# Kernel tuning notes

Hardware: AMD Instinct MI355X
Metric: run time of the kernel (lower is better)

## Reference

```python
import jax, jax.numpy as jnp
import numpy as np

D_MODEL = 768
N_HEADS = 12
HEAD_DIM = D_MODEL // N_HEADS


def setup_inputs() -> dict:
    key = jax.random.key(0)
    ks = jax.random.split(key, 7)
    B, S = 4, 2048
    scale = 1.0 / np.sqrt(D_MODEL)
    return {
        "hidden_states": jax.random.normal(ks[0], (B, S, D_MODEL), dtype=jnp.float32),
        "attention_mask": jnp.ones((B, S), dtype=jnp.float32),
        "Wq": jax.random.normal(ks[1], (D_MODEL, D_MODEL), dtype=jnp.float32) * scale,
        "bq": jnp.zeros((D_MODEL,), dtype=jnp.float32),
        "Wk": jax.random.normal(ks[2], (D_MODEL, D_MODEL), dtype=jnp.float32) * scale,
        "bk": jnp.zeros((D_MODEL,), dtype=jnp.float32),
        "Wv": jax.random.normal(ks[3], (D_MODEL, D_MODEL), dtype=jnp.float32) * scale,
        "bv": jnp.zeros((D_MODEL,), dtype=jnp.float32),
    }


def reference(hidden_states, attention_mask, Wq, bq, Wk, bk, Wv, bv):
    B, S, _ = hidden_states.shape

    def heads(x):  # [B,S,D] -> [B,H,S,hd]
        return x.reshape(B, S, N_HEADS, HEAD_DIM).transpose(0, 2, 1, 3)

    q = heads(hidden_states @ Wq + bq)
    k = heads(hidden_states @ Wk + bk)
    v = heads(hidden_states @ Wv + bv)

    # [B,H,S,S] scores -- explicitly materialized, as in the original module
    scores = jnp.einsum("bhqd,bhkd->bhqk", q, k) / np.sqrt(HEAD_DIM)
    mask_add = (1.0 - attention_mask)[:, None, None, :] * -10000.0
    scores = scores + mask_add
    probs = jax.nn.softmax(scores, axis=-1)  # dropout p=0 (eval) -> identity

    ctx = jnp.einsum("bhqk,bhkd->bhqd", probs, v)
    ctx = ctx.transpose(0, 2, 1, 3).reshape(B, S, D_MODEL)
    return ctx, probs
```

## Files before the change

### kernel.cpp

```cpp
#include <hip/hip_runtime.h>
#include <hip/hip_bf16.h>
#include <cstdint>

typedef short bf16x8 __attribute__((ext_vector_type(8)));
typedef float f32x4 __attribute__((ext_vector_type(4)));
typedef unsigned short ushort_t;

__device__ __forceinline__ ushort_t f2bf(float f) {
    uint32_t u = __float_as_uint(f);
    u = (u + 0x7fffu + ((u >> 16) & 1u)) >> 16;
    return (ushort_t)u;
}

__device__ __forceinline__ ushort_t f2bf_native(float f) {
    __hip_bfloat16 h = __float2bfloat16(f);
    return *reinterpret_cast<ushort_t*>(&h);
}

__device__ __forceinline__ void gl2lds16(const void* g, void* l) {
    __builtin_amdgcn_global_load_lds((const __attribute__((address_space(1))) void*)(g),
                                     (__attribute__((address_space(3))) void*)(l), 16, 0, 0);
}

__device__ __forceinline__ void wait_vm0() {
    asm volatile("s_waitcnt vmcnt(0)" ::: "memory");
}
__device__ __forceinline__ void wait_vm8() {
    asm volatile("s_waitcnt vmcnt(8)" ::: "memory");
}

__global__ void cvt_hidden(const float* __restrict__ in, ushort_t* __restrict__ out, int n4) {
    int i = blockIdx.x * blockDim.x + threadIdx.x;
    for (; i < n4; i += gridDim.x * blockDim.x) {
        float4 v = ((const float4*)in)[i];
        ushort_t tmp[4] __attribute__((aligned(8)));
        tmp[0] = f2bf(v.x); tmp[1] = f2bf(v.y); tmp[2] = f2bf(v.z); tmp[3] = f2bf(v.w);
        ((uint2*)out)[i] = *(uint2*)tmp;
    }
}

__global__ void wt_transpose(const float* __restrict__ Wq, const float* __restrict__ Wk,
                             const float* __restrict__ Wv, ushort_t* __restrict__ out) {
    __shared__ float tile[64][68];
    const float* W = blockIdx.z == 0 ? Wq : (blockIdx.z == 1 ? Wk : Wv);
    int k0 = blockIdx.x * 64, n0 = blockIdx.y * 64;
    int t = threadIdx.x;
    for (int i = 0; i < 4; ++i) {
        int e = i * 1024 + t * 4;
        int r = e >> 6, c = e & 63;
        float4 v = *(const float4*)(W + (k0 + r) * 768 + n0 + c);
        *(float4*)(&tile[r][c]) = v;
    }
    __syncthreads();
    ushort_t* o = out + blockIdx.z * 768 * 768;
    for (int i = 0; i < 2; ++i) {
        int e = i * 2048 + t * 8;
        int rn = e >> 6, ck = e & 63;
        ushort_t tmp[8] __attribute__((aligned(16)));
        for (int j = 0; j < 8; ++j) tmp[j] = f2bf(tile[ck + j][rn]);
        *(int4*)(o + (n0 + rn) * 768 + k0 + ck) = *(int4*)tmp;
    }
}

__launch_bounds__(256, 2)
__global__ void qkv_gemm(const ushort_t* __restrict__ A, const ushort_t* __restrict__ Wt,
                         const float* __restrict__ bq, const float* __restrict__ bk,
                         const float* __restrict__ bv,
                         ushort_t* __restrict__ q_out, ushort_t* __restrict__ k_out,
                         ushort_t* __restrict__ vt_out) {
    __shared__ char smem[65536];
    char* sA = smem;
    char* sB = smem + 32768;
    int z = blockIdx.z;
    const ushort_t* Wz = Wt + z * 589824;
    const float* bias = z == 0 ? bq : (z == 1 ? bk : bv);
    int m0 = blockIdx.x * 128, n0 = blockIdx.y * 128;
    int t = threadIdx.x, lane = t & 63, w = t >> 6;
    int wr = w >> 1, wc = w & 1;
    int lr = lane & 15, lg = lane >> 4;
    int rsub = lane >> 3;
    int jsw  = ((lane & 7) ^ rsub) * 8;

#pragma unroll
    for (int i = 0; i < 4; ++i) {
        int r = i * 32 + w * 8 + rsub;
        gl2lds16(A + (m0 + r) * 768 + jsw, sA + i * 4096 + w * 1024);
        gl2lds16(Wz + (n0 + r) * 768 + jsw, sB + i * 4096 + w * 1024);
    }
    wait_vm0();
    __syncthreads();

    f32x4 acc[4][4] = {};
    int cur = 0;
    for (int ktile = 0; ktile < 12; ++ktile) {
        char* sAc = sA + cur * 16384;
        char* sBc = sB + cur * 16384;
        if (ktile < 11) {
            char* sAn = sA + (cur ^ 1) * 16384;
            char* sBn = sB + (cur ^ 1) * 16384;
            int kt = (ktile + 1) * 64;
#pragma unroll
            for (int i = 0; i < 4; ++i) {
                int r = i * 32 + w * 8 + rsub;
                gl2lds16(A + (m0 + r) * 768 + kt + jsw, sAn + i * 4096 + w * 1024);
                gl2lds16(Wz + (n0 + r) * 768 + kt + jsw, sBn + i * 4096 + w * 1024);
            }
        }
        bf16x8 af[2][4], bfr[2][4];
#pragma unroll
        for (int kf = 0; kf < 2; ++kf)
#pragma unroll
            for (int mf = 0; mf < 4; ++mf) {
                int row = wr * 64 + mf * 16 + lr;
                af[kf][mf] = *(const bf16x8*)(sAc + ((row * 128 + (kf * 32 + lg * 8) * 2) ^ ((row & 7) << 4)));
            }
#pragma unroll
        for (int kf = 0; kf < 2; ++kf)
#pragma unroll
            for (int nf = 0; nf < 4; ++nf) {
                int row = wc * 64 + nf * 16 + lr;
                bfr[kf][nf] = *(const bf16x8*)(sBc + ((row * 128 + (kf * 32 + lg * 8) * 2) ^ ((row & 7) << 4)));
            }
        __builtin_amdgcn_s_setprio(1);
#pragma unroll
        for (int kf = 0; kf < 2; ++kf)
#pragma unroll
            for (int mf = 0; mf < 4; ++mf)
#pragma unroll
                for (int nf = 0; nf < 4; ++nf)
                    acc[mf][nf] = __builtin_amdgcn_mfma_f32_16x16x32_bf16(af[kf][mf], bfr[kf][nf], acc[mf][nf], 0, 0, 0);
        __builtin_amdgcn_s_setprio(0);
        wait_vm0();
        __syncthreads();
        cur ^= 1;
    }
    if (z == 2) {
        for (int nf = 0; nf < 4; ++nf) {
            int n = n0 + wc * 64 + nf * 16 + lr;
            float bv_ = bias[n];
            int h = n >> 6, d = n & 63;
            for (int mf = 0; mf < 4; ++mf) {
                int m = m0 + wr * 64 + mf * 16 + lg * 4;
                int b = m >> 11, s = m & 2047;
                ushort_t tmp[4] __attribute__((aligned(8)));
                for (int rr = 0; rr < 4; ++rr) tmp[rr] = f2bf(acc[mf][nf][rr] + bv_);
                *(uint2*)(vt_out + ((size_t)(b * 12 + h) * 64 + d) * 2048 + s) = *(uint2*)tmp;
            }
        }
    } else {
        ushort_t* outp = z == 0 ? q_out : k_out;
        float scale = z == 0 ? 0.125f : 1.0f;
        for (int nf = 0; nf < 4; ++nf) {
            int n = n0 + wc * 64 + nf * 16 + lr;
            float bv_ = bias[n];
            int h = n >> 6, d = n & 63;
            for (int mf = 0; mf < 4; ++mf) {
                for (int rr = 0; rr < 4; ++rr) {
                    int m = m0 + wr * 64 + mf * 16 + lg * 4 + rr;
                    float val = (acc[mf][nf][rr] + bv_) * scale;
                    int b = m >> 11, s = m & 2047;
                    outp[((b * 12 + h) * 2048 + s) * 64 + d] = f2bf(val);
                }
            }
        }
    }
}

__launch_bounds__(256, 3)
__global__ void attn_fused(const ushort_t* __restrict__ qs, const ushort_t* __restrict__ ks,
                           const ushort_t* __restrict__ vt, const float* __restrict__ mask,
                           float* __restrict__ ctx, float* __restrict__ probs) {
    __shared__ char smem[49152];
    char* sK = smem;
    char* sV = smem + 16384;
    char* sP = smem + 32768;
    int id = blockIdx.x;
    int nid = (id & 7) * 96 + (id >> 3);
    int qt = nid & 15, bh = nid >> 4;
    int b = bh / 12, h = bh % 12;
    int q0 = qt * 128;
    int t = threadIdx.x, lane = t & 63, w = t >> 6;
    int lr = lane & 15, lg = lane >> 4;
    const ushort_t* Qb = qs + bh * 131072;
    const ushort_t* Kb = ks + bh * 131072;
    const ushort_t* Vb = vt + bh * 131072;
    const float* mb = mask + b * 2048;
    float* prow = probs + (size_t)bh * 4194304;

    int rsub = lane >> 3;
    int jsw  = ((lane & 7) ^ rsub) * 8;

#pragma unroll
    for (int i = 0; i < 4; ++i) {
        int r = i * 32 + w * 8 + rsub;
        gl2lds16(Qb + (q0 + r) * 64 + jsw, sK + i * 4096 + w * 1024);
    }
    wait_vm0();
    __syncthreads();
    bf16x8 qa[2][2];
#pragma unroll
    for (int mf = 0; mf < 2; ++mf)
#pragma unroll
        for (int kf = 0; kf < 2; ++kf) {
            int row = w * 32 + mf * 16 + lr;
            qa[mf][kf] = *(const bf16x8*)(sK + ((row * 128 + (kf * 32 + lg * 8) * 2) ^ ((row & 7) << 4)));
        }
    __syncthreads();

#pragma unroll
    for (int t2 = 0; t2 < 2; ++t2)
#pragma unroll
        for (int i = 0; i < 2; ++i) {
            int r = t2 * 64 + i * 32 + w * 8 + rsub;
            gl2lds16(Kb + r * 64 + jsw, smem + t2 * 8192 + i * 4096 + w * 1024);
        }
    wait_vm0();
    __syncthreads();
    float lsum[2] = {0.f, 0.f};
    int cur = 0;
    for (int kp = 0; kp < 16; ++kp) {
        char* bufc = smem + cur * 16384;
        if (kp < 15) {
            char* bufn = smem + (cur ^ 1) * 16384;
#pragma unroll
            for (int t2 = 0; t2 < 2; ++t2)
#pragma unroll
                for (int i = 0; i < 2; ++i) {
                    int r = ((kp + 1) * 2 + t2) * 64 + i * 32 + w * 8 + rsub;
                    gl2lds16(Kb + r * 64 + jsw, bufn + t2 * 8192 + i * 4096 + w * 1024);
                }
        }
#pragma unroll
        for (int t2 = 0; t2 < 2; ++t2) {
            int kt = kp * 2 + t2;
            char* sKc = bufc + t2 * 8192;
#pragma unroll
            for (int n16 = 0; n16 < 4; ++n16) {
                int krow = n16 * 16 + lr;
                bf16x8 kb0 = *(const bf16x8*)(sKc + ((krow * 128 + (lg * 8) * 2) ^ ((krow & 7) << 4)));
                bf16x8 kb1 = *(const bf16x8*)(sKc + ((krow * 128 + (32 + lg * 8) * 2) ^ ((krow & 7) << 4)));
                float4 m4 = *(const float4*)(mb + kt * 64 + n16 * 16 + lg * 4);
                float ma0 = (1.0f - m4.x) * -10000.0f;
                float ma1 = (1.0f - m4.y) * -10000.0f;
                float ma2 = (1.0f - m4.z) * -10000.0f;
                float ma3 = (1.0f - m4.w) * -10000.0f;
#pragma unroll
                for (int mf = 0; mf < 2; ++mf) {
                    f32x4 sacc = {};
                    sacc = __builtin_amdgcn_mfma_f32_16x16x32_bf16(kb0, qa[mf][0], sacc, 0, 0, 0);
                    sacc = __builtin_amdgcn_mfma_f32_16x16x32_bf16(kb1, qa[mf][1], sacc, 0, 0, 0);
                    lsum[mf] += (__expf(sacc[0] + ma0) + __expf(sacc[1] + ma1))
                              + (__expf(sacc[2] + ma2) + __expf(sacc[3] + ma3));
                }
            }
        }
        wait_vm0();
        __syncthreads();
        cur ^= 1;
    }
#pragma unroll
    for (int mf = 0; mf < 2; ++mf) {
        lsum[mf] += __shfl_xor(lsum[mf], 16);
        lsum[mf] += __shfl_xor(lsum[mf], 32);
    }
    float inv2[2] = {1.0f / lsum[0], 1.0f / lsum[1]};

#pragma unroll
    for (int i = 0; i < 2; ++i) {
        int r = i * 32 + w * 8 + rsub;
        gl2lds16(Kb + r * 64 + jsw, sK + i * 4096 + w * 1024);
        gl2lds16(Vb + r * 2048 + jsw, sV + i * 4096 + w * 1024);
    }
    wait_vm0();
    __syncthreads();

    f32x4 oacc[2][4] = {};
    cur = 0;
    for (int kt = 0; kt < 32; ++kt) {
        char* sKc = sK + cur * 8192;
        char* sVc = sV + cur * 8192;
        if (kt < 31) {
            char* sKn = sK + (cur ^ 1) * 8192;
            char* sVn = sV + (cur ^ 1) * 8192;
            int nt = kt + 1;
#pragma unroll
            for (int i = 0; i < 2; ++i) {
                int r = i * 32 + w * 8 + rsub;
                gl2lds16(Kb + (nt * 64 + r) * 64 + jsw, sKn + i * 4096 + w * 1024);
                gl2lds16(Vb + r * 2048 + nt * 64 + jsw, sVn + i * 4096 + w * 1024);
            }
        }
#pragma unroll
        for (int n16 = 0; n16 < 4; ++n16) {
            int krow = n16 * 16 + lr;
            bf16x8 kb0 = *(const bf16x8*)(sKc + ((krow * 128 + (lg * 8) * 2) ^ ((krow & 7) << 4)));
            bf16x8 kb1 = *(const bf16x8*)(sKc + ((krow * 128 + (32 + lg * 8) * 2) ^ ((krow & 7) << 4)));
            float4 m4 = *(const float4*)(mb + kt * 64 + n16 * 16 + lg * 4);
            float ma0 = (1.0f - m4.x) * -10000.0f;
            float ma1 = (1.0f - m4.y) * -10000.0f;
            float ma2 = (1.0f - m4.z) * -10000.0f;
            float ma3 = (1.0f - m4.w) * -10000.0f;
#pragma unroll
            for (int mf = 0; mf < 2; ++mf) {
                f32x4 sacc = {};
                sacc = __builtin_amdgcn_mfma_f32_16x16x32_bf16(kb0, qa[mf][0], sacc, 0, 0, 0);
                sacc = __builtin_amdgcn_mfma_f32_16x16x32_bf16(kb1, qa[mf][1], sacc, 0, 0, 0);
                ushort_t tmp[4] __attribute__((aligned(8)));
                tmp[0] = f2bf_native(__expf(sacc[0] + ma0) * inv2[mf]);
                tmp[1] = f2bf_native(__expf(sacc[1] + ma1) * inv2[mf]);
                tmp[2] = f2bf_native(__expf(sacc[2] + ma2) * inv2[mf]);
                tmp[3] = f2bf_native(__expf(sacc[3] + ma3) * inv2[mf]);
                *(uint2*)(sP + w * 4096 + mf * 2048 +
                          ((lr * 128 + n16 * 32 + lg * 8) ^ ((lr & 7) << 4))) = *(uint2*)tmp;
            }
        }
#pragma unroll
        for (int mf = 0; mf < 2; ++mf)
#pragma unroll
            for (int step = 0; step < 4; ++step) {
                int srow = step * 4 + lg;
                uint2 uu = *(const uint2*)(sP + w * 4096 + mf * 2048 +
                                           ((srow * 128 + lr * 8) ^ ((srow & 7) << 4)));
                f32x4 pv;
                pv[0] = __uint_as_float((uu.x & 0xffffu) << 16);
                pv[1] = __uint_as_float(uu.x & 0xffff0000u);
                pv[2] = __uint_as_float((uu.y & 0xffffu) << 16);
                pv[3] = __uint_as_float(uu.y & 0xffff0000u);
                *(f32x4*)(prow + (size_t)(q0 + w * 32 + mf * 16 + srow) * 2048 + kt * 64 + lr * 4) = pv;
            }
        __builtin_amdgcn_s_setprio(1);
#pragma unroll
        for (int mf = 0; mf < 2; ++mf)
#pragma unroll
            for (int kf = 0; kf < 2; ++kf) {
                bf16x8 pa = *(const bf16x8*)(sP + w * 4096 + mf * 2048 +
                                             ((lr * 128 + (kf * 32 + lg * 8) * 2) ^ ((lr & 7) << 4)));
#pragma unroll
                for (int dt = 0; dt < 4; ++dt) {
                    int vrow = dt * 16 + lr;
                    bf16x8 vb = *(const bf16x8*)(sVc + ((vrow * 128 + (kf * 32 + lg * 8) * 2) ^ ((vrow & 7) << 4)));
                    oacc[mf][dt] = __builtin_amdgcn_mfma_f32_16x16x32_bf16(pa, vb, oacc[mf][dt], 0, 0, 0);
                }
            }
        __builtin_amdgcn_s_setprio(0);
        wait_vm8();
        __syncthreads();
        cur ^= 1;
    }
#pragma unroll
    for (int mf = 0; mf < 2; ++mf)
#pragma unroll
        for (int dt = 0; dt < 4; ++dt)
#pragma unroll
            for (int r = 0; r < 4; ++r) {
                int qabs = q0 + w * 32 + mf * 16 + lg * 4 + r;
                ctx[(size_t)(b * 2048 + qabs) * 768 + h * 64 + dt * 16 + lr] = oacc[mf][dt][r];
            }
}

extern "C" void kernel_launch(void* const* d_in, const int* in_sizes, int n_in,
                              void* d_out, int out_size, void* d_ws, size_t ws_size,
                              hipStream_t stream) {
    const float* hidden = (const float*)d_in[0];
    const float* mask   = (const float*)d_in[1];
    const float* Wq     = (const float*)d_in[2];
    const float* bq     = (const float*)d_in[3];
    const float* Wk     = (const float*)d_in[4];
    const float* bk     = (const float*)d_in[5];
    const float* Wv     = (const float*)d_in[6];
    const float* bv     = (const float*)d_in[7];
    float* ctx   = (float*)d_out;
    float* probs = ctx + 6291456;

    char* ws = (char*)d_ws;
    ushort_t* hidB = (ushort_t*)(ws);
    ushort_t* WtB  = (ushort_t*)(ws + 12582912);
    ushort_t* qsB  = (ushort_t*)(ws + 16121856);
    ushort_t* ksB  = (ushort_t*)(ws + 28704768);
    ushort_t* vtB  = (ushort_t*)(ws + 41287680);

    hipLaunchKernelGGL(cvt_hidden, dim3(6144), dim3(256), 0, stream, hidden, hidB, 1572864);
    hipLaunchKernelGGL(wt_transpose, dim3(12, 12, 3), dim3(256), 0, stream, Wq, Wk, Wv, WtB);
    hipLaunchKernelGGL(qkv_gemm, dim3(64, 6, 3), dim3(256), 0, stream,
                       hidB, WtB, bq, bk, bv, qsB, ksB, vtB);
    hipLaunchKernelGGL(attn_fused, dim3(768), dim3(256), 0, stream, qsB, ksB, vtB, mask, ctx, probs);
}
```

Baseline: 265.6 us.

## Merge prep kernels and read V straight from global into registers

The hidden-state bf16 conversion and the weight transpose kernels are folded into one launch with a block-index split, which saves a kernel launch and its tail. In the attention kernel's second pass, V tiles are no longer double-buffered through LDS with async global-to-LDS copies. Each lane now loads its V fragments directly from global memory into registers at the start of every key tile. This removes LDS traffic and V-slot bookkeeping, but V load latency is now hidden only by the QK and softmax work within the same iteration. The V loads also share the vmcnt queue with the probs stores, so waits may get longer.

```diff
diff --git a/kernel.cpp b/kernel.cpp
--- a/kernel.cpp
+++ b/kernel.cpp
@@ -29,36 +29,36 @@
     asm volatile("s_waitcnt vmcnt(8)" ::: "memory");
 }
 
-__global__ void cvt_hidden(const float* __restrict__ in, ushort_t* __restrict__ out, int n4) {
-    int i = blockIdx.x * blockDim.x + threadIdx.x;
-    for (; i < n4; i += gridDim.x * blockDim.x) {
-        float4 v = ((const float4*)in)[i];
+__global__ void prep(const float* __restrict__ hidden, const float* __restrict__ Wq,
+                     const float* __restrict__ Wk, const float* __restrict__ Wv,
+                     ushort_t* __restrict__ hidB, ushort_t* __restrict__ WtB) {
+    __shared__ float tile[64][68];
+    int id = blockIdx.x, t = threadIdx.x;
+    if (id < 432) {
+        int x = id % 12, y = (id / 12) % 12, z = id / 144;
+        const float* W = z == 0 ? Wq : (z == 1 ? Wk : Wv);
+        int k0 = x * 64, n0 = y * 64;
+        for (int i = 0; i < 4; ++i) {
+            int e = i * 1024 + t * 4;
+            int r = e >> 6, c = e & 63;
+            float4 v = *(const float4*)(W + (k0 + r) * 768 + n0 + c);
+            *(float4*)(&tile[r][c]) = v;
+        }
+        __syncthreads();
+        ushort_t* o = WtB + z * 589824;
+        for (int i = 0; i < 2; ++i) {
+            int e = i * 2048 + t * 8;
+            int rn = e >> 6, ck = e & 63;
+            ushort_t tmp[8] __attribute__((aligned(16)));
+            for (int j = 0; j < 8; ++j) tmp[j] = f2bf(tile[ck + j][rn]);
+            *(int4*)(o + (n0 + rn) * 768 + k0 + ck) = *(int4*)tmp;
+        }
+    } else {
+        int i = (id - 432) * 256 + t;
+        float4 v = ((const float4*)hidden)[i];
         ushort_t tmp[4] __attribute__((aligned(8)));
         tmp[0] = f2bf(v.x); tmp[1] = f2bf(v.y); tmp[2] = f2bf(v.z); tmp[3] = f2bf(v.w);
-        ((uint2*)out)[i] = *(uint2*)tmp;
-    }
-}
-
-__global__ void wt_transpose(const float* __restrict__ Wq, const float* __restrict__ Wk,
-                             const float* __restrict__ Wv, ushort_t* __restrict__ out) {
-    __shared__ float tile[64][68];
-    const float* W = blockIdx.z == 0 ? Wq : (blockIdx.z == 1 ? Wk : Wv);
-    int k0 = blockIdx.x * 64, n0 = blockIdx.y * 64;
-    int t = threadIdx.x;
-    for (int i = 0; i < 4; ++i) {
-        int e = i * 1024 + t * 4;
-        int r = e >> 6, c = e & 63;
-        float4 v = *(const float4*)(W + (k0 + r) * 768 + n0 + c);
-        *(float4*)(&tile[r][c]) = v;
-    }
-    __syncthreads();
-    ushort_t* o = out + blockIdx.z * 768 * 768;
-    for (int i = 0; i < 2; ++i) {
-        int e = i * 2048 + t * 8;
-        int rn = e >> 6, ck = e & 63;
-        ushort_t tmp[8] __attribute__((aligned(16)));
-        for (int j = 0; j < 8; ++j) tmp[j] = f2bf(tile[ck + j][rn]);
-        *(int4*)(o + (n0 + rn) * 768 + k0 + ck) = *(int4*)tmp;
+        ((uint2*)hidB)[i] = *(uint2*)tmp;
     }
 }
 
@@ -172,7 +172,6 @@
                            float* __restrict__ ctx, float* __restrict__ probs) {
     __shared__ char smem[49152];
     char* sK = smem;
-    char* sV = smem + 16384;
     char* sP = smem + 32768;
     int id = blockIdx.x;
     int nid = (id & 7) * 96 + (id >> 3);
@@ -269,7 +268,6 @@
     for (int i = 0; i < 2; ++i) {
         int r = i * 32 + w * 8 + rsub;
         gl2lds16(Kb + r * 64 + jsw, sK + i * 4096 + w * 1024);
-        gl2lds16(Vb + r * 2048 + jsw, sV + i * 4096 + w * 1024);
     }
     wait_vm0();
     __syncthreads();
@@ -278,16 +276,19 @@
     cur = 0;
     for (int kt = 0; kt < 32; ++kt) {
         char* sKc = sK + cur * 8192;
-        char* sVc = sV + cur * 8192;
+        bf16x8 vreg[2][4];
+#pragma unroll
+        for (int kf = 0; kf < 2; ++kf)
+#pragma unroll
+            for (int dt = 0; dt < 4; ++dt)
+                vreg[kf][dt] = *(const bf16x8*)(Vb + (dt * 16 + lr) * 2048 + kt * 64 + kf * 32 + lg * 8);
         if (kt < 31) {
             char* sKn = sK + (cur ^ 1) * 8192;
-            char* sVn = sV + (cur ^ 1) * 8192;
             int nt = kt + 1;
 #pragma unroll
             for (int i = 0; i < 2; ++i) {
                 int r = i * 32 + w * 8 + rsub;
                 gl2lds16(Kb + (nt * 64 + r) * 64 + jsw, sKn + i * 4096 + w * 1024);
-                gl2lds16(Vb + r * 2048 + nt * 64 + jsw, sVn + i * 4096 + w * 1024);
             }
         }
 #pragma unroll
@@ -336,11 +337,8 @@
                 bf16x8 pa = *(const bf16x8*)(sP + w * 4096 + mf * 2048 +
                                              ((lr * 128 + (kf * 32 + lg * 8) * 2) ^ ((lr & 7) << 4)));
 #pragma unroll
-                for (int dt = 0; dt < 4; ++dt) {
-                    int vrow = dt * 16 + lr;
-                    bf16x8 vb = *(const bf16x8*)(sVc + ((vrow * 128 + (kf * 32 + lg * 8) * 2) ^ ((vrow & 7) << 4)));
-                    oacc[mf][dt] = __builtin_amdgcn_mfma_f32_16x16x32_bf16(pa, vb, oacc[mf][dt], 0, 0, 0);
-                }
+                for (int dt = 0; dt < 4; ++dt)
+                    oacc[mf][dt] = __builtin_amdgcn_mfma_f32_16x16x32_bf16(pa, vreg[kf][dt], oacc[mf][dt], 0, 0, 0);
             }
         __builtin_amdgcn_s_setprio(0);
         wait_vm8();
@@ -379,8 +377,7 @@
     ushort_t* ksB  = (ushort_t*)(ws + 28704768);
     ushort_t* vtB  = (ushort_t*)(ws + 41287680);
 
-    hipLaunchKernelGGL(cvt_hidden, dim3(6144), dim3(256), 0, stream, hidden, hidB, 1572864);
-    hipLaunchKernelGGL(wt_transpose, dim3(12, 12, 3), dim3(256), 0, stream, Wq, Wk, Wv, WtB);
+    hipLaunchKernelGGL(prep, dim3(6576), dim3(256), 0, stream, hidden, Wq, Wk, Wv, hidB, WtB);
     hipLaunchKernelGGL(qkv_gemm, dim3(64, 6, 3), dim3(256), 0, stream,
                        hidB, WtB, bq, bk, bv, qsB, ksB, vtB);
     hipLaunchKernelGGL(attn_fused, dim3(768), dim3(256), 0, stream, qsB, ksB, vtB, mask, ctx, probs);
```

Measured after the change: 330.4 us. 1.24x slower.
